# Kernel tuning notes

Measured on AMD Instinct MI355X. Metric: run time of the kernel, lower is better.

## Reference

```python
import jax, jax.numpy as jnp
import numpy as np

N_QUBIT = 14
N_LAYER = 16
BATCH = 512
DIM = 2 ** N_QUBIT

# wire 0 is the most-significant bit (deepquantum convention: state.reshape([2]*n), wire i = axis i)
_bits = (np.arange(DIM)[:, None] >> (N_QUBIT - 1 - np.arange(N_QUBIT))) & 1
SIGNS = jnp.asarray(2.0 * _bits - 1.0, dtype=jnp.float32)  # (DIM, n_qubit), -1 for bit=0, +1 for bit=1


def _apply_1q(state, gate, w):
    # state: (B, DIM) complex64; gate: (2,2) complex
    B = state.shape[0]
    left, right = 2 ** w, 2 ** (N_QUBIT - w - 1)
    st = state.reshape(B, left, 2, right)
    return jnp.einsum('ab,xlbr->xlar', gate, st).reshape(B, DIM)


def _cnot(state, c, t):
    # CNOT control c, target t: X on target where control bit = 1
    B = state.shape[0]
    st = state.reshape((B,) + (2,) * N_QUBIT)
    ax_c, ax_t = c + 1, t + 1
    a0 = jnp.take(st, 0, axis=ax_c)
    a1 = jnp.take(st, 1, axis=ax_c)
    a1 = jnp.flip(a1, axis=ax_t if ax_t < ax_c else ax_t - 1)  # flip size-2 axis == X gate
    return jnp.stack([a0, a1], axis=ax_c).reshape(B, DIM)


def _rz_layer(state, thetas):
    # RZ(th) = diag(e^{-i th/2}, e^{+i th/2}) on every wire -> single fused diagonal phase
    return state * jnp.exp(0.5j * (SIGNS @ thetas))


def _ry_layer(state, thetas):
    for w in range(N_QUBIT):
        c = jnp.cos(thetas[w] * 0.5)
        s = jnp.sin(thetas[w] * 0.5)
        gate = jnp.stack([jnp.stack([c, -s]), jnp.stack([s, c])]).astype(jnp.complex64)
        state = _apply_1q(state, gate, w)
    return state


def _circuit(z, theta):
    state = z.reshape(z.shape[0], DIM)
    for l in range(N_LAYER):
        state = _rz_layer(state, theta[l, 0])
        state = _ry_layer(state, theta[l, 1])
        state = _rz_layer(state, theta[l, 2])
        for w in range(N_QUBIT):  # cnot_ring
            state = _cnot(state, w, (w + 1) % N_QUBIT)
    return state


def _split(state, w):
    B = state.shape[0]
    st = state.reshape(B, 2 ** w, 2, 2 ** (N_QUBIT - w - 1))
    return st[:, :, 0, :], st[:, :, 1, :]


def _expectations(state):
    outs = []
    for w in (0, 1):  # <Z_w> = sum |psi_0|^2 - |psi_1|^2
        p0, p1 = _split(state, w)
        outs.append(jnp.sum(jnp.abs(p0) ** 2 - jnp.abs(p1) ** 2, axis=(1, 2)))
    cross0 = None
    for w in (0, 1):  # <X_w> = 2 Re sum conj(psi_0) psi_1
        p0, p1 = _split(state, w)
        cr = jnp.conj(p0) * p1
        if w == 0:
            cross0 = cr
        outs.append(2.0 * jnp.sum(jnp.real(cr), axis=(1, 2)))
    outs.append(2.0 * jnp.sum(jnp.imag(cross0), axis=(1, 2)))  # <Y_0> = 2 Im sum conj(psi_0) psi_1
    return jnp.stack(outs, axis=1).astype(jnp.float32)  # (B, 5)


def setup_inputs() -> dict:
    key = jax.random.key(0)
    k1, k2, k3, k4 = jax.random.split(key, 4)
    zr = jax.random.normal(k1, (BATCH, DIM), dtype=jnp.float32)
    zi = jax.random.normal(k2, (BATCH, DIM), dtype=jnp.float32)
    z = (zr + 1j * zi).astype(jnp.complex64)
    z = z / jnp.linalg.norm(z, axis=1, keepdims=True)  # normalized quantum states
    z = z[:, :, None]  # (B, 2^n, 1) per docstring
    theta = jax.random.normal(k3, (N_LAYER, 3, N_QUBIT), dtype=jnp.float32)
    y = jax.random.randint(k4, (BATCH,), 0, 5)
    return {"z": z, "theta": theta, "y": y}


def reference(z, theta, y):
    state = _circuit(z, theta)
    output = _expectations(state)
    logp = jax.nn.log_softmax(output, axis=1)
    loss = -jnp.mean(jnp.take_along_axis(logp, y[:, None], axis=1))
    return (loss, output)
```

## Files before the change

### kernel.cpp

```cpp
#include <hip/hip_runtime.h>
#include <hip/hip_bf16.h>

#define NQ     14
#define DIM    16384
#define NLAYER 16
#define BATCH  512
#define NT     1024

typedef float v2f __attribute__((ext_vector_type(2)));

__device__ __forceinline__ constexpr int POSB(int x){ return (x ^ ((x >> 5) & 31)) << 3; }

__device__ __forceinline__ float bf2f(unsigned int u16){
  union { unsigned int i; float f; } v; v.i = u16 << 16; return v.f;
}

__device__ __forceinline__ float thv(const void* th, int i, bool b16){
  return b16 ? bf2f(((const unsigned short*)th)[i]) : ((const float*)th)[i];
}

__device__ int srcF(int x){
  int v = x;
  #pragma unroll
  for (int k = 13; k >= 0; --k){
    int tb = 13 - ((k + 1) % 14);
    v ^= ((v >> (13 - k)) & 1) << tb;
  }
  return v;
}

__device__ __forceinline__ v2f cmul(v2f a, v2f b){
  v2f t, d;
  asm("v_pk_mul_f32 %0, %1, %2 op_sel:[0,0] op_sel_hi:[1,0]"
      : "=v"(t) : "v"(a), "v"(b));
  asm("v_pk_fma_f32 %0, %1, %2, %3 op_sel:[1,1,0] op_sel_hi:[0,1,1] neg_lo:[0,1,0]"
      : "=v"(d) : "v"(a), "v"(b), "v"(t));
  return d;
}

__device__ __forceinline__ void rot2(v2f& a0, v2f& a1, float c, float s){
  v2f c2 = (v2f){c, c}, s2 = (v2f){s, s};
  v2f t0 = a0;
  a0 = a0 * c2 - a1 * s2;
  a1 = t0 * s2 + a1 * c2;
}

__global__ __launch_bounds__(NT) __attribute__((amdgpu_waves_per_eu(4, 4)))
void qnn_circuit(const void* __restrict__ zraw,
                 const void* __restrict__ theta,
                 float* __restrict__ out)
{
  __shared__ v2f   S[DIM];
  __shared__ v2f   ph0H[128], ph0L[128], ph2H[128], ph2L[128];
  __shared__ float csT[28];
  __shared__ int   sHB[128], sLB[128];
  __shared__ float red[16*5];

  char* Sb = (char*)S;
  const int t = threadIdx.x;
  const int b = blockIdx.x;

  int pred = 0;
  if (t < 336){
    unsigned int w  = ((const unsigned int*)theta)[t];
    unsigned int lo = w & 0xffffu;
    unsigned int e  = (lo >> 7) & 0xffu;
    pred = (e >= 100 && e <= 140) || (lo == 0);
  }
  const bool th_b16 = (__syncthreads_count(pred) > 250);

  pred = 0;
  if (t < 256){
    unsigned int w  = ((const unsigned int*)zraw)[t];
    unsigned int lo = w & 0xffffu;
    unsigned int e  = (lo >> 7) & 0xffu;
    pred = (e >= 88 && e <= 140) || (lo == 0);
  }
  const bool z_b16 = (__syncthreads_count(pred) > 160);

  if (t < 128){ sHB[t] = POSB(srcF(t << 7)); sLB[t] = POSB(srcF(t)); }

  if (z_b16){
    const uint4* zb = (const uint4*)((const unsigned short*)zraw + (size_t)b * (DIM * 2));
    #pragma unroll 1
    for (int jj = 0; jj < 4; ++jj){
      int x4 = t + NT * jj;
      uint4 w = zb[x4];
      int xb = x4 * 4;
      *(v2f*)(Sb + POSB(xb+0)) = (v2f){bf2f(w.x & 0xffffu), bf2f(w.x >> 16)};
      *(v2f*)(Sb + POSB(xb+1)) = (v2f){bf2f(w.y & 0xffffu), bf2f(w.y >> 16)};
      *(v2f*)(Sb + POSB(xb+2)) = (v2f){bf2f(w.z & 0xffffu), bf2f(w.z >> 16)};
      *(v2f*)(Sb + POSB(xb+3)) = (v2f){bf2f(w.w & 0xffffu), bf2f(w.w >> 16)};
    }
  } else {
    const float4* zf = (const float4*)((const float*)zraw + (size_t)b * DIM);
    #pragma unroll 1
    for (int jj = 0; jj < 4; ++jj){
      int x4 = t + NT * jj;
      float4 w = zf[x4];
      int xb = x4 * 4;
      *(v2f*)(Sb + POSB(xb+0)) = (v2f){w.x, 0.f};
      *(v2f*)(Sb + POSB(xb+1)) = (v2f){w.y, 0.f};
      *(v2f*)(Sb + POSB(xb+2)) = (v2f){w.z, 0.f};
      *(v2f*)(Sb + POSB(xb+3)) = (v2f){w.w, 0.f};
    }
  }
  __syncthreads();

  const int pwb = POSB(t);
  const int hb  = t >> 7;
  const int slB = sLB[t & 127];

  const int pb2 = POSB(((t >> 7) << 10) | (t & 127));
  const int pb3 = POSB(((t >> 7) << 10) | (((t >> 5) & 1) << 9)
                     | (((t >> 4) & 1) << 8) | (((t >> 6) & 1) << 7) | (t & 15));
  const int pb4 = POSB(((t >> 8) << 10) | (((t >> 4) & 1) << 9) | (((t >> 3) & 1) << 8)
                     | (((t >> 2) & 1) << 7) | (((t >> 6) & 1) << 6) | (((t >> 5) & 1) << 5)
                     | (((t >> 7) & 1) << 4) | (t & 3));
  const int x5base = ((t >> 8) << 10) | ((t & 31) << 5) | (((t >> 7) & 1) << 4)
                   | (((t >> 6) & 1) << 3) | (((t >> 5) & 1) << 2);
  const int pb5 = POSB(x5base);
  const int lb5 = x5base & 127;

  for (int l = 0; l < NLAYER; ++l){
    const int thb = l * 42;

    if (t < 512){
      int grp = t >> 7, idx = t & 127;
      int tz = thb + ((grp >= 2) ? 28 : 0);
      float ph = 0.f;
      if ((grp & 1) == 0){
        #pragma unroll
        for (int w = 0; w < 7; ++w)
          ph += (((idx >> (6 - w)) & 1) ? 0.5f : -0.5f) * thv(theta, tz + w, th_b16);
      } else {
        #pragma unroll
        for (int w = 7; w < 14; ++w)
          ph += (((idx >> (13 - w)) & 1) ? 0.5f : -0.5f) * thv(theta, tz + w, th_b16);
      }
      float sn, cs; sincosf(ph, &sn, &cs);
      v2f v = (v2f){cs, sn};
      if      (grp == 0) ph0H[idx] = v;
      else if (grp == 1) ph0L[idx] = v;
      else if (grp == 2) ph2H[idx] = v;
      else               ph2L[idx] = v;
    } else if (t < 512 + 14){
      int q = t - 512;
      float sn, cs; sincosf(0.5f * thv(theta, thb + 14 + q, th_b16), &sn, &cs);
      csT[2*q] = cs; csT[2*q+1] = sn;
    }

    {
      v2f g[16];
      if (l == 0){
        #pragma unroll
        for (int j = 0; j < 16; ++j) g[j] = *(v2f*)(Sb + (pwb ^ (j << 13)));
      } else {
        #pragma unroll
        for (int j = 0; j < 16; ++j)
          g[j] = *(v2f*)(Sb + (sHB[hb + 8*j] ^ slB));
      }
      __syncthreads();

      {
        v2f cl = ph0L[t & 127];
        #pragma unroll
        for (int j = 0; j < 16; ++j)
          g[j] = cmul(g[j], cmul(ph0H[hb + 8*j], cl));
      }
      #pragma unroll
      for (int q = 0; q < 4; ++q){
        float c = csT[2*q], sn = csT[2*q+1];
        int m = 8 >> q;
        #pragma unroll
        for (int j = 0; j < 16; ++j){
          if (j & m) continue;
          rot2(g[j], g[j | m], c, sn);
        }
      }
      #pragma unroll
      for (int j = 0; j < 16; ++j) *(v2f*)(Sb + (pwb ^ (j << 13))) = g[j];
    }
    __syncthreads();

    #pragma unroll 1
    for (int it = 0; it < 2; ++it){
      int pb = pb2 ^ (it << 16);
      v2f h[8];
      #pragma unroll
      for (int j = 0; j < 8; ++j) h[j] = *(v2f*)(Sb + (pb ^ (((j << 7) | (j << 2)) << 3)));
      #pragma unroll
      for (int q = 0; q < 3; ++q){
        float c = csT[2*(4+q)], sn = csT[2*(4+q)+1];
        int m = 4 >> q;
        #pragma unroll
        for (int j = 0; j < 8; ++j){
          if (j & m) continue;
          rot2(h[j], h[j | m], c, sn);
        }
      }
      #pragma unroll
      for (int j = 0; j < 8; ++j) *(v2f*)(Sb + (pb ^ (((j << 7) | (j << 2)) << 3))) = h[j];
    }
    __syncthreads();

    #pragma unroll 1
    for (int it = 0; it < 2; ++it){
      int pb = pb3 ^ (it << 16);
      v2f h[8];
      #pragma unroll
      for (int j = 0; j < 8; ++j) h[j] = *(v2f*)(Sb + (pb ^ (((j << 4) | (j >> 1)) << 3)));
      #pragma unroll
      for (int q = 0; q < 3; ++q){
        float c = csT[2*(7+q)], sn = csT[2*(7+q)+1];
        int m = 4 >> q;
        #pragma unroll
        for (int j = 0; j < 8; ++j){
          if (j & m) continue;
          rot2(h[j], h[j | m], c, sn);
        }
      }
      #pragma unroll
      for (int j = 0; j < 8; ++j) *(v2f*)(Sb + (pb ^ (((j << 4) | (j >> 1)) << 3))) = h[j];
    }
    __syncthreads();

    #pragma unroll 1
    for (int it = 0; it < 4; ++it){
      int pb = pb4 ^ (it << 15);
      v2f h[4];
      #pragma unroll
      for (int j = 0; j < 4; ++j) h[j] = *(v2f*)(Sb + (pb ^ (j << 5)));
      #pragma unroll
      for (int q = 0; q < 2; ++q){
        float c = csT[2*(10+q)], sn = csT[2*(10+q)+1];
        int m = 2 >> q;
        #pragma unroll
        for (int j = 0; j < 4; ++j){
          if (j & m) continue;
          rot2(h[j], h[j | m], c, sn);
        }
      }
      #pragma unroll
      for (int j = 0; j < 4; ++j) *(v2f*)(Sb + (pb ^ (j << 5))) = h[j];
    }
    __syncthreads();

    #pragma unroll 1
    for (int it = 0; it < 4; ++it){
      int pb = pb5 ^ (it << 15);
      v2f h[4];
      #pragma unroll
      for (int j = 0; j < 4; ++j) h[j] = *(v2f*)(Sb + (pb ^ (j << 3)));
      #pragma unroll
      for (int q = 0; q < 2; ++q){
        float c = csT[2*(12+q)], sn = csT[2*(12+q)+1];
        int m = 2 >> q;
        #pragma unroll
        for (int j = 0; j < 4; ++j){
          if (j & m) continue;
          rot2(h[j], h[j | m], c, sn);
        }
      }
      {
        v2f chh = ph2H[(x5base >> 7) | (it << 5)];
        #pragma unroll
        for (int j = 0; j < 4; ++j)
          h[j] = cmul(h[j], cmul(chh, ph2L[lb5 | j]));
      }
      #pragma unroll
      for (int j = 0; j < 4; ++j) *(v2f*)(Sb + (pb ^ (j << 3))) = h[j];
    }
    __syncthreads();
  }

  float z0=0.f, z1=0.f, x0s=0.f, x1s=0.f, y0s=0.f;
  {
    v2f g[16];
    #pragma unroll
    for (int j = 0; j < 16; ++j)
      g[j] = *(v2f*)(Sb + (sHB[hb + 8*j] ^ slB));

    #pragma unroll
    for (int j = 0; j < 16; ++j){
      float pw = g[j].x*g[j].x + g[j].y*g[j].y;
      z0 += (j & 8) ? -pw : pw;
      z1 += (j & 4) ? -pw : pw;
    }
    #pragma unroll
    for (int j = 0; j < 8; ++j){
      v2f p0 = g[j], p1 = g[j+8];
      x0s += 2.f*(p0.x*p1.x + p0.y*p1.y);
      y0s += 2.f*(p0.x*p1.y - p0.y*p1.x);
    }
    #pragma unroll
    for (int j = 0; j < 16; ++j){
      if (j & 4) continue;
      v2f p0 = g[j], p1 = g[j|4];
      x1s += 2.f*(p0.x*p1.x + p0.y*p1.y);
    }
  }
  #pragma unroll
  for (int o = 32; o >= 1; o >>= 1){
    z0  += __shfl_down(z0,  o, 64);
    z1  += __shfl_down(z1,  o, 64);
    x0s += __shfl_down(x0s, o, 64);
    x1s += __shfl_down(x1s, o, 64);
    y0s += __shfl_down(y0s, o, 64);
  }
  int wid = t >> 6, lane = t & 63;
  if (lane == 0){
    red[wid*5+0]=z0; red[wid*5+1]=z1; red[wid*5+2]=x0s; red[wid*5+3]=x1s; red[wid*5+4]=y0s;
  }
  __syncthreads();
  if (t < 5){
    float sum = 0.f;
    #pragma unroll
    for (int w = 0; w < 16; ++w) sum += red[w*5 + t];
    out[1 + b*5 + t] = sum;
  }
}

__global__ __launch_bounds__(512)
void qnn_loss(const int* __restrict__ y, float* __restrict__ out)
{
  __shared__ float red[8];
  int t = threadIdx.x;
  const float* o = out + 1 + t*5;
  float o0=o[0], o1=o[1], o2=o[2], o3=o[3], o4=o[4];
  float m = fmaxf(fmaxf(fmaxf(o0,o1), fmaxf(o2,o3)), o4);
  float sum = expf(o0-m)+expf(o1-m)+expf(o2-m)+expf(o3-m)+expf(o4-m);
  float lse = m + logf(sum);
  int yi = y[t]; yi = yi < 0 ? 0 : (yi > 4 ? 4 : yi);
  float lb = lse - o[yi];

  #pragma unroll
  for (int ofs = 32; ofs >= 1; ofs >>= 1) lb += __shfl_down(lb, ofs, 64);
  if ((t & 63) == 0) red[t >> 6] = lb;
  __syncthreads();
  if (t == 0){
    float s = 0.f;
    #pragma unroll
    for (int w = 0; w < 8; ++w) s += red[w];
    out[0] = s / (float)BATCH;
  }
}

extern "C" void kernel_launch(void* const* d_in, const int* in_sizes, int n_in,
                              void* d_out, int out_size, void* d_ws, size_t ws_size,
                              hipStream_t stream)
{
  const void* z     = d_in[0];
  const void* theta = d_in[1];
  const int*  y     = (const int*)d_in[2];
  float*      out   = (float*)d_out;

  qnn_circuit<<<BATCH, NT, 0, stream>>>(z, theta, out);
  qnn_loss<<<1, 512, 0, stream>>>(y, out);
}
```

Measured before the change: 305.1 us.

## Merge last two RY sub-passes into one 16-element register pass per thread

Replaces the two 4-iteration passes over the low four qubits (wires 10-13) with one pass. In it, each thread loads 16 contiguous amplitudes, applies all four rotations and the following RZ phase in registers, then writes them back. This removes one full LDS read/write sweep of the state and one __syncthreads per layer. In exchange it raises register pressure to 16 complex values per thread and changes the LDS access pattern, which could add bank conflicts under the swizzle.

```diff
diff --git a/kernel.cpp b/kernel.cpp
--- a/kernel.cpp
+++ b/kernel.cpp
@@ -114,13 +114,9 @@
   const int pb2 = POSB(((t >> 7) << 10) | (t & 127));
   const int pb3 = POSB(((t >> 7) << 10) | (((t >> 5) & 1) << 9)
                      | (((t >> 4) & 1) << 8) | (((t >> 6) & 1) << 7) | (t & 15));
-  const int pb4 = POSB(((t >> 8) << 10) | (((t >> 4) & 1) << 9) | (((t >> 3) & 1) << 8)
-                     | (((t >> 2) & 1) << 7) | (((t >> 6) & 1) << 6) | (((t >> 5) & 1) << 5)
-                     | (((t >> 7) & 1) << 4) | (t & 3));
-  const int x5base = ((t >> 8) << 10) | ((t & 31) << 5) | (((t >> 7) & 1) << 4)
-                   | (((t >> 6) & 1) << 3) | (((t >> 5) & 1) << 2);
-  const int pb5 = POSB(x5base);
-  const int lb5 = x5base & 127;
+  const int pbM = POSB(t << 4);
+  const int lbM = (t & 7) << 4;
+  const int hbM = t >> 3;
 
   for (int l = 0; l < NLAYER; ++l){
     const int thb = l * 42;
@@ -225,51 +221,28 @@
     }
     __syncthreads();
 
-    #pragma unroll 1
-    for (int it = 0; it < 4; ++it){
-      int pb = pb4 ^ (it << 15);
-      v2f h[4];
-      #pragma unroll
-      for (int j = 0; j < 4; ++j) h[j] = *(v2f*)(Sb + (pb ^ (j << 5)));
-      #pragma unroll
-      for (int q = 0; q < 2; ++q){
+    {
+      v2f h[16];
+      #pragma unroll
+      for (int j = 0; j < 16; ++j) h[j] = *(v2f*)(Sb + (pbM ^ (j << 3)));
+      #pragma unroll
+      for (int q = 0; q < 4; ++q){
         float c = csT[2*(10+q)], sn = csT[2*(10+q)+1];
-        int m = 2 >> q;
-        #pragma unroll
-        for (int j = 0; j < 4; ++j){
+        int m = 8 >> q;
+        #pragma unroll
+        for (int j = 0; j < 16; ++j){
           if (j & m) continue;
           rot2(h[j], h[j | m], c, sn);
         }
       }
-      #pragma unroll
-      for (int j = 0; j < 4; ++j) *(v2f*)(Sb + (pb ^ (j << 5))) = h[j];
-    }
-    __syncthreads();
-
-    #pragma unroll 1
-    for (int it = 0; it < 4; ++it){
-      int pb = pb5 ^ (it << 15);
-      v2f h[4];
-      #pragma unroll
-      for (int j = 0; j < 4; ++j) h[j] = *(v2f*)(Sb + (pb ^ (j << 3)));
-      #pragma unroll
-      for (int q = 0; q < 2; ++q){
-        float c = csT[2*(12+q)], sn = csT[2*(12+q)+1];
-        int m = 2 >> q;
-        #pragma unroll
-        for (int j = 0; j < 4; ++j){
-          if (j & m) continue;
-          rot2(h[j], h[j | m], c, sn);
-        }
-      }
       {
-        v2f chh = ph2H[(x5base >> 7) | (it << 5)];
-        #pragma unroll
-        for (int j = 0; j < 4; ++j)
-          h[j] = cmul(h[j], cmul(chh, ph2L[lb5 | j]));
-      }
-      #pragma unroll
-      for (int j = 0; j < 4; ++j) *(v2f*)(Sb + (pb ^ (j << 3))) = h[j];
+        v2f chh = ph2H[hbM];
+        #pragma unroll
+        for (int j = 0; j < 16; ++j)
+          h[j] = cmul(h[j], cmul(chh, ph2L[lbM | j]));
+      }
+      #pragma unroll
+      for (int j = 0; j < 16; ++j) *(v2f*)(Sb + (pbM ^ (j << 3))) = h[j];
     }
     __syncthreads();
   }
```

New measurement: 344.3 us. 1.13x slower.
